# Optimization experiments

Measured on AMD Instinct MI355X. Metric: run time of the kernel, lower is better.

Reference implementation:

```python
import jax, jax.numpy as jnp
import numpy as np
import math

B, S, D, H = 4, 1024, 1024, 16
DK = D // H


def setup_inputs() -> dict:
    key = jax.random.key(0)
    ks = jax.random.split(key, 13)
    s = 1.0 / math.sqrt(D)
    inp = {
        "query": jax.random.normal(ks[0], (B, S, D), jnp.float32),
        "key": jax.random.normal(ks[1], (B, S, D), jnp.float32),
        "value": jax.random.normal(ks[2], (B, S, D), jnp.float32),
        "mask": jax.random.randint(ks[3], (B, S, S), 0, 2, jnp.int32),
        "wq": jax.random.normal(ks[4], (D, D), jnp.float32) * s,
        "bq": jax.random.normal(ks[5], (D,), jnp.float32) * s,
        "wk": jax.random.normal(ks[6], (D, D), jnp.float32) * s,
        "bk": jax.random.normal(ks[7], (D,), jnp.float32) * s,
        "wv": jax.random.normal(ks[8], (D, D), jnp.float32) * s,
        "bv": jax.random.normal(ks[9], (D,), jnp.float32) * s,
        "wo": jax.random.normal(ks[10], (D, D), jnp.float32) * s,
        "bo": jax.random.normal(ks[11], (D,), jnp.float32) * s,
    }
    return inp


def reference(query, key, value, mask, wq, bq, wk, bk, wv, bv, wo, bo):
    # QKV projections, split into heads: [B,S,D] -> [B,H,S,DK]
    def proj(x, w, b):
        return (x @ w.T + b).reshape(B, S, H, DK).transpose(0, 2, 1, 3)

    q = proj(query, wq, bq)
    k = proj(key, wk, bk)
    v = proj(value, wv, bv)

    scores = jnp.einsum("bhqd,bhkd->bhqk", q, k) / math.sqrt(DK)
    scores = scores + mask[:, None, :, :].astype(scores.dtype) * (-1e9)
    p = jax.nn.softmax(scores, axis=-1)
    x = jnp.einsum("bhqk,bhkd->bhqd", p, v)
    x = x.transpose(0, 2, 1, 3).reshape(B, S, D)
    # output projection (dropout is identity in eval)
    return x @ wo.T + bo
```

## Files before the change

kernel.cpp:

```cpp
#include <hip/hip_runtime.h>
#include <hip/hip_bf16.h>


typedef __bf16 bf16x8 __attribute__((ext_vector_type(8)));
typedef float f32x4 __attribute__((ext_vector_type(4)));
typedef unsigned short us8 __attribute__((ext_vector_type(8)));
typedef unsigned short us4 __attribute__((ext_vector_type(4)));

#define MFMA(a, b, c) __builtin_amdgcn_mfma_f32_16x16x32_bf16(a, b, c, 0, 0, 0)
#define EXP2(x) __builtin_amdgcn_exp2f(x)

__device__ __forceinline__ unsigned short f2b(float f) {
  return __builtin_bit_cast(unsigned short, __float2bfloat16(f));
}
__device__ __forceinline__ float b2f(unsigned short u) {
  return __builtin_bit_cast(float, (unsigned)u << 16);
}
__device__ __forceinline__ unsigned cvtpk(float lo, float hi) {
  unsigned r;
  asm("v_cvt_pk_bf16_f32 %0, %1, %2" : "=v"(r) : "v"(lo), "v"(hi));
  return r;
}
__device__ __forceinline__ bf16x8 ldbf8(const unsigned short* p) {
  return __builtin_bit_cast(bf16x8, *reinterpret_cast<const us8*>(p));
}
__device__ __forceinline__ us8 cvt8(float4 a, float4 b) {
  us8 o;
  o[0] = f2b(a.x); o[1] = f2b(a.y); o[2] = f2b(a.z); o[3] = f2b(a.w);
  o[4] = f2b(b.x); o[5] = f2b(b.y); o[6] = f2b(b.z); o[7] = f2b(b.w);
  return o;
}
__device__ __forceinline__ void glds16(const void* g, void* l) {
  __builtin_amdgcn_global_load_lds(
      (const __attribute__((address_space(1))) unsigned int*)g,
      (__attribute__((address_space(3))) unsigned int*)l, 16, 0, 0);
}

__global__ __launch_bounds__(256)
void prep(const float* __restrict__ query, const float* __restrict__ key,
          const float* __restrict__ value, const float* __restrict__ wq,
          const float* __restrict__ wk, const float* __restrict__ wv,
          unsigned short* __restrict__ Abfq, unsigned short* __restrict__ Abfk,
          unsigned short* __restrict__ Abfv, unsigned short* __restrict__ Wb) {
  const int bid = blockIdx.x, tid = threadIdx.x;
  const float* src;
  unsigned short* dst;
  size_t off;
  if (bid < 1536) {
    const int widx = bid >> 9;
    src = (widx == 0) ? wq : (widx == 1) ? wk : wv;
    dst = Wb + (size_t)widx * 1048576;
    off = (size_t)(bid & 511) * 2048 + tid * 8;
  } else if (bid < 3584) {
    src = query; dst = Abfq; off = (size_t)(bid - 1536) * 2048 + tid * 8;
  } else if (bid < 5632) {
    src = key; dst = Abfk; off = (size_t)(bid - 3584) * 2048 + tid * 8;
  } else {
    src = value; dst = Abfv; off = (size_t)(bid - 5632) * 2048 + tid * 8;
  }
  const float4* p = reinterpret_cast<const float4*>(src + off);
  *reinterpret_cast<us8*>(dst + off) = cvt8(p[0], p[1]);
}

__global__ __launch_bounds__(256)
void maskcvt(const int* __restrict__ mask, unsigned short* __restrict__ Mf) {
  const int idx = blockIdx.x * 256 + threadIdx.x;
  const int wl = idx & 63, tile = idx >> 6;
  const int kt = tile & 63, qt = (tile >> 6) & 63, b = tile >> 12;
  const int lr = wl & 15, lg = wl >> 4;
  const int4 mv = *reinterpret_cast<const int4*>(
      mask + (size_t)(b * 1024 + qt * 16 + lr) * 1024 + kt * 16 + lg * 4);
  us4 o;
  o[0] = mv.x ? 0xCEACu : 0xC1C0u;
  o[1] = mv.y ? 0xCEACu : 0xC1C0u;
  o[2] = mv.z ? 0xCEACu : 0xC1C0u;
  o[3] = mv.w ? 0xCEACu : 0xC1C0u;
  *reinterpret_cast<us4*>(Mf + (size_t)idx * 4) = o;
}

__global__ __launch_bounds__(256)
void cvt_w(const float* __restrict__ src, unsigned short* __restrict__ dst) {
  const size_t off = (size_t)blockIdx.x * 2048 + threadIdx.x * 8;
  const float4* p = reinterpret_cast<const float4*>(src + off);
  *reinterpret_cast<us8*>(dst + off) = cvt8(p[0], p[1]);
}

__global__ __launch_bounds__(256, 6)
void gemm_proj(const unsigned short* __restrict__ Aq,
               const unsigned short* __restrict__ Ak,
               const unsigned short* __restrict__ Av_bf,
               const float* __restrict__ Av_f32,
               const unsigned short* __restrict__ Wb,
               const float* __restrict__ bq, const float* __restrict__ bk,
               const float* __restrict__ bv, unsigned short* __restrict__ Qb,
               unsigned short* __restrict__ Kf, unsigned short* __restrict__ Vf,
               float qscale) {
  constexpr int K = 1024, N = 1024;
  __shared__ __align__(16) unsigned short As[2][128 * 32];
  __shared__ __align__(16) unsigned short Bs[2][64 * 32];
  const int lid = blockIdx.x + (blockIdx.y << 5) + (blockIdx.z << 9);
  const int xcd = lid & 7, slot = lid >> 3;
  const int chunk = ((slot >> 4) << 3) + xcd;
  const int z = chunk >> 5;
  const int bm = (chunk & 31) * 128;
  const int bn = (slot & 15) * 64;

  const unsigned short* Abf = (z == 0) ? Aq : (z == 1) ? Ak : Av_bf;
  const bool f32path = (z == 2) && (Av_bf == nullptr);
  const unsigned short* Bw = Wb + (size_t)z * 1048576;
  const float* bias = (z == 0) ? bq : (z == 1) ? bk : bv;
  const int t = threadIdx.x;
  const int w = t >> 6, lane = t & 63, lr = lane & 15, lg = lane >> 4;
  const int wr = w >> 1, wc = w & 1;

#define SWZ(row) ((((row) ^ ((row) >> 2)) & 3) << 4)

  f32x4 acc[4][2];
#pragma unroll
  for (int m = 0; m < 4; ++m)
#pragma unroll
    for (int n = 0; n < 2; ++n) acc[m][n] = f32x4{0.f, 0.f, 0.f, 0.f};

  auto stageA = [&](int k0, int buf) {
#pragma unroll
    for (int it = 0; it < 2; ++it) {
      const int s = it * 256 + t, row = s >> 2, cb = (s & 3) * 16;
      const char* g = (const char*)Abf + ((size_t)(bm + row) * 1024 + k0) * 2 +
                      (cb ^ SWZ(row));
      char* l = (char*)&As[buf][0] + (it * 256 + w * 64) * 16;
      glds16(g, l);
    }
  };
  auto stageB = [&](int k0, int buf) {
    const int row = t >> 2, cb = (t & 3) * 16;
    const char* g = (const char*)Bw + ((size_t)(bn + row) * 1024 + k0) * 2 +
                    (cb ^ SWZ(row));
    char* l = (char*)&Bs[buf][0] + (w * 64) * 16;
    glds16(g, l);
  };
#define STA8(buf, it, v)                                                       \
  {                                                                            \
    const int s_ = (it) * 256 + t, row_ = s_ >> 2, cb_ = (s_ & 3) * 16;        \
    *reinterpret_cast<us8*>((char*)&As[buf][0] + row_ * 64 +                   \
                            (cb_ ^ SWZ(row_))) = (v);                          \
  }

  if (f32path) {
#pragma unroll
    for (int it = 0; it < 2; ++it) {
      const int s = it * 256 + t, row = s >> 2, col = (s & 3) * 8;
      const float4* p =
          reinterpret_cast<const float4*>(Av_f32 + (size_t)(bm + row) * K + col);
      STA8(0, it, cvt8(p[0], p[1]));
    }
  } else {
    stageA(0, 0);
  }
  stageB(0, 0);
  __syncthreads();

  for (int c = 0; c < 32; ++c) {
    const int buf = c & 1;
    float4 fa[4];
    if (c < 31) {
      const int k1 = (c + 1) * 32;
      if (f32path) {
#pragma unroll
        for (int it = 0; it < 2; ++it) {
          const int s = it * 256 + t, row = s >> 2, col = (s & 3) * 8;
          const float4* p = reinterpret_cast<const float4*>(
              Av_f32 + (size_t)(bm + row) * K + k1 + col);
          fa[2 * it] = p[0];
          fa[2 * it + 1] = p[1];
        }
      } else {
        stageA(k1, buf ^ 1);
      }
      stageB(k1, buf ^ 1);
    }
    {
      bf16x8 af[4], bfr[2];
#pragma unroll
      for (int m = 0; m < 4; ++m) {
        const int row = wr * 64 + m * 16 + lr;
        af[m] = ldbf8((const unsigned short*)((char*)&As[buf][0] + row * 64 +
                                              ((lg * 16) ^ SWZ(row))));
      }
#pragma unroll
      for (int n = 0; n < 2; ++n) {
        const int row = wc * 32 + n * 16 + lr;
        bfr[n] = ldbf8((const unsigned short*)((char*)&Bs[buf][0] + row * 64 +
                                               ((lg * 16) ^ SWZ(row))));
      }
#pragma unroll
      for (int m = 0; m < 4; ++m)
#pragma unroll
        for (int n = 0; n < 2; ++n) acc[m][n] = MFMA(af[m], bfr[n], acc[m][n]);
    }
    if (c < 31 && f32path) {
#pragma unroll
      for (int it = 0; it < 2; ++it) STA8(buf ^ 1, it, cvt8(fa[2 * it], fa[2 * it + 1]));
    }
    __syncthreads();
  }
#undef STA8
#undef SWZ

#pragma unroll
  for (int m = 0; m < 4; ++m) {
    const int mr = bm + wr * 64 + m * 16 + lg * 4;
#pragma unroll
    for (int nt = 0; nt < 2; ++nt) {
      const int n = bn + wc * 32 + nt * 16 + lr;
      const float bb = bias[n];
      if (z == 0) {
#pragma unroll
        for (int r = 0; r < 4; ++r)
          Qb[(size_t)(mr + r) * N + n] = f2b((acc[m][nt][r] + bb) * qscale);
      } else if (z == 1) {
        const int b2 = mr >> 10, s0 = mr & 1023, hh = n >> 6, dd = n & 63;
        const size_t base = (size_t)(b2 * 16 + hh) * 65536 + (size_t)(dd >> 5) * 32768 +
                            (size_t)(s0 >> 4) * 512 +
                            (size_t)((s0 & 15) | (((dd >> 3) & 3) << 4)) * 8 + (dd & 7);
#pragma unroll
        for (int r = 0; r < 4; ++r) Kf[base + r * 8] = f2b(acc[m][nt][r] + bb);
      } else {
        const int b2 = mr >> 10, s0 = mr & 1023, hh = n >> 6, dd = n & 63;
        const size_t base = (size_t)(b2 * 16 + hh) * 65536 + (size_t)(s0 >> 5) * 2048 +
                            (size_t)(dd >> 4) * 512 +
                            (size_t)((dd & 15) | (((s0 >> 3) & 3) << 4)) * 8 + (s0 & 7);
        us4 pk;
#pragma unroll
        for (int r = 0; r < 4; ++r) pk[r] = f2b(acc[m][nt][r] + bb);
        *reinterpret_cast<us4*>(&Vf[base]) = pk;
      }
    }
  }
}

__global__ __launch_bounds__(256)
void gemm_out(const unsigned short* __restrict__ A, const unsigned short* __restrict__ Bw,
              const float* __restrict__ bias, float* __restrict__ Out) {
  constexpr int K = 1024, N = 1024;
  __shared__ __align__(16) unsigned short As[2][128 * 64];
  __shared__ __align__(16) unsigned short Bs[2][64 * 64];
  const int lid = blockIdx.x + (blockIdx.y << 5);
  const int xcd = lid & 7, slot = lid >> 3;
  const int chunk = ((slot >> 5) << 3) + xcd;
  const int pos = slot & 31;
  const int bm = ((chunk << 1) + (pos >> 4)) * 128;
  const int bn = (pos & 15) * 64;
  const int t = threadIdx.x;
  const int w = t >> 6, lane = t & 63, lr = lane & 15, lg = lane >> 4;
  const int wr = w >> 1, wc = w & 1;
  const int swzc = (lr & 7) << 4;

  f32x4 acc[4][2];
#pragma unroll
  for (int m = 0; m < 4; ++m)
#pragma unroll
    for (int n = 0; n < 2; ++n) acc[m][n] = f32x4{0.f, 0.f, 0.f, 0.f};

  auto stageA = [&](int k0, int buf) {
#pragma unroll
    for (int it = 0; it < 4; ++it) {
      const int s = it * 256 + t, row = s >> 3, cb = (s & 7) * 16;
      const char* g = (const char*)A + ((size_t)(bm + row) * 1024 + k0) * 2 +
                      (cb ^ ((row & 7) << 4));
      char* l = (char*)&As[buf][0] + (it * 256 + w * 64) * 16;
      glds16(g, l);
    }
  };
  auto stageB = [&](int k0, int buf) {
#pragma unroll
    for (int it = 0; it < 2; ++it) {
      const int s = it * 256 + t, row = s >> 3, cb = (s & 7) * 16;
      const char* g = (const char*)Bw + ((size_t)(bn + row) * 1024 + k0) * 2 +
                      (cb ^ ((row & 7) << 4));
      char* l = (char*)&Bs[buf][0] + (it * 256 + w * 64) * 16;
      glds16(g, l);
    }
  };

  stageA(0, 0);
  stageB(0, 0);
  __syncthreads();

  for (int c = 0; c < 16; ++c) {
    const int buf = c & 1;
    if (c < 15) {
      const int k1 = (c + 1) * 64;
      stageA(k1, buf ^ 1);
      stageB(k1, buf ^ 1);
    }
#pragma unroll
    for (int h2 = 0; h2 < 2; ++h2) {
      bf16x8 af[4], bfr[2];
#pragma unroll
      for (int m = 0; m < 4; ++m) {
        const int row = wr * 64 + m * 16 + lr;
        af[m] = ldbf8((const unsigned short*)((char*)&As[buf][0] + row * 128 +
                                              ((h2 * 64 + lg * 16) ^ swzc)));
      }
#pragma unroll
      for (int n = 0; n < 2; ++n) {
        const int row = wc * 32 + n * 16 + lr;
        bfr[n] = ldbf8((const unsigned short*)((char*)&Bs[buf][0] + row * 128 +
                                               ((h2 * 64 + lg * 16) ^ swzc)));
      }
#pragma unroll
      for (int m = 0; m < 4; ++m)
#pragma unroll
        for (int n = 0; n < 2; ++n) acc[m][n] = MFMA(af[m], bfr[n], acc[m][n]);
    }
    __syncthreads();
  }

#pragma unroll
  for (int m = 0; m < 4; ++m) {
    const int mr = bm + wr * 64 + m * 16 + lg * 4;
#pragma unroll
    for (int nt = 0; nt < 2; ++nt) {
      const int n = bn + wc * 32 + nt * 16 + lr;
      const float bb = bias[n];
#pragma unroll
      for (int r = 0; r < 4; ++r) Out[(size_t)(mr + r) * N + n] = acc[m][nt][r] + bb;
    }
  }
}

__global__ __launch_bounds__(256)
void attn_v7(const unsigned short* __restrict__ Qb,
             const unsigned short* __restrict__ Kf,
             const unsigned short* __restrict__ Vf,
             const unsigned short* __restrict__ Mf,
             unsigned short* __restrict__ ctx) {
  __shared__ __align__(16) unsigned short S[2][8192];
  __shared__ __align__(16) unsigned short sP[4][16 * 64];
  const int lid = blockIdx.x + (blockIdx.y << 6);
  const int xcd = lid & 7, slot = lid >> 3;
  const int bh = ((slot >> 4) << 3) + xcd;
  const int qb = slot & 15;
  const int b = bh >> 4, h = bh & 15;
  const int t = threadIdx.x, w = t >> 6, wl = t & 63, lr = wl & 15, lg = wl >> 4;
  const int q0 = qb * 64 + w * 16;
  const int swz = (lr & 7) << 4;

  const unsigned short* qp = Qb + (size_t)(b * 1024 + q0 + lr) * 1024 + h * 64 + lg * 8;
  const bf16x8 bq0 = ldbf8(qp);
  const bf16x8 bq1 = ldbf8(qp + 32);

  const unsigned short* KfB = Kf + (size_t)bh * 65536;
  const unsigned short* VfB = Vf + (size_t)bh * 65536;
  const unsigned short* mfp = Mf + (size_t)((b * 64 + qb * 4 + w) * 64) * 256 + wl * 4;

  f32x4 O[4];
  float l_ = 0.f;
#pragma unroll
  for (int dt = 0; dt < 4; ++dt) O[dt] = f32x4{0.f, 0.f, 0.f, 0.f};
  unsigned short* sp = &sP[w][0];

  auto stage = [&](int kc, int buf) {
    const unsigned short* srcs[4] = {KfB + kc * 2048, KfB + 32768 + kc * 2048,
                                     VfB + kc * 4096, VfB + kc * 4096 + 2048};
#pragma unroll
    for (int r = 0; r < 4; ++r) {
      const char* g = (const char*)(srcs[r] + (size_t)t * 8);
      char* l = (char*)&S[buf][r * 2048 + w * 512];
      glds16(g, l);
    }
  };

  stage(0, 0);
  __syncthreads();

  for (int kc = 0; kc < 16; ++kc) {
    const int buf = kc & 1;
    if (kc < 15) stage(kc + 1, buf ^ 1);

    us4 mk[4];
#pragma unroll
    for (int t4 = 0; t4 < 4; ++t4)
      mk[t4] = *reinterpret_cast<const us4*>(mfp + (size_t)(kc * 4 + t4) * 256);

    bf16x8 ak[4][2];
#pragma unroll
    for (int t4 = 0; t4 < 4; ++t4) {
      ak[t4][0] = ldbf8(&S[buf][t4 * 512 + wl * 8]);
      ak[t4][1] = ldbf8(&S[buf][2048 + t4 * 512 + wl * 8]);
    }

    f32x4 sc[4];
    __builtin_amdgcn_s_setprio(1);
#pragma unroll
    for (int t4 = 0; t4 < 4; ++t4) {
      f32x4 a;
#pragma unroll
      for (int r = 0; r < 4; ++r) a[r] = b2f(mk[t4][r]);
      a = MFMA(ak[t4][0], bq0, a);
      a = MFMA(ak[t4][1], bq1, a);
      sc[t4] = a;
    }
    __builtin_amdgcn_s_setprio(0);

    float ps = 0.f;
#pragma unroll
    for (int t4 = 0; t4 < 4; ++t4) {
      const float e0 = EXP2(sc[t4][0]), e1 = EXP2(sc[t4][1]);
      const float e2 = EXP2(sc[t4][2]), e3 = EXP2(sc[t4][3]);
      ps += (e0 + e1) + (e2 + e3);
      uint2 pw;
      pw.x = cvtpk(e0, e1);
      pw.y = cvtpk(e2, e3);
      *reinterpret_cast<uint2*>((char*)sp + lr * 128 + ((t4 * 32 + lg * 8) ^ swz)) = pw;
    }
    ps += __shfl_xor(ps, 16);
    ps += __shfl_xor(ps, 32);
    l_ += ps;

    __builtin_amdgcn_s_setprio(1);
#pragma unroll
    for (int ks = 0; ks < 2; ++ks) {
      bf16x8 ap =
          ldbf8((const unsigned short*)((char*)sp + lr * 128 + ((ks * 64 + lg * 16) ^ swz)));
#pragma unroll
      for (int dt = 0; dt < 4; ++dt) {
        bf16x8 bv = ldbf8(&S[buf][4096 + ks * 2048 + dt * 512 + wl * 8]);
        O[dt] = MFMA(ap, bv, O[dt]);
      }
    }
    __builtin_amdgcn_s_setprio(0);

    __syncthreads();
  }

  float linv[4];
#pragma unroll
  for (int r = 0; r < 4; ++r) linv[r] = 1.0f / __shfl(l_, lg * 4 + r);
#pragma unroll
  for (int dt = 0; dt < 4; ++dt)
#pragma unroll
    for (int r = 0; r < 4; ++r)
      ctx[(size_t)(b * 1024 + q0 + lg * 4 + r) * 1024 + h * 64 + dt * 16 + lr] =
          f2b(O[dt][r] * linv[r]);
}

extern "C" void kernel_launch(void* const* d_in, const int* in_sizes, int n_in,
                              void* d_out, int out_size, void* d_ws, size_t ws_size,
                              hipStream_t stream) {
  const float* query = (const float*)d_in[0];
  const float* key   = (const float*)d_in[1];
  const float* value = (const float*)d_in[2];
  const int*   mask  = (const int*)d_in[3];
  const float* wq = (const float*)d_in[4];
  const float* bq = (const float*)d_in[5];
  const float* wk = (const float*)d_in[6];
  const float* bk = (const float*)d_in[7];
  const float* wv = (const float*)d_in[8];
  const float* bv = (const float*)d_in[9];
  const float* wo = (const float*)d_in[10];
  const float* bo = (const float*)d_in[11];
  float* out = (float*)d_out;

  const size_t SZ = (size_t)4096 * 1024;
  unsigned short* Qb   = (unsigned short*)d_ws;
  unsigned short* Kf   = Qb + SZ;
  unsigned short* Vf   = Kf + SZ;
  unsigned short* ctx  = Vf + SZ;
  unsigned short* Abfq = (unsigned short*)d_out;
  unsigned short* Wb   = Abfq + SZ;
  unsigned short* Mf   = (unsigned short*)d_out;
  unsigned short* Abfk = ctx;
  const bool big = ws_size >= (size_t)40 * 1024 * 1024;
  unsigned short* Abfv = big ? (ctx + SZ) : nullptr;
  unsigned short* Wob  = Vf;

  const float qscale = 0.125f * 1.4426950408889634f;
  dim3 blk(256);
  prep<<<big ? 7680 : 5632, blk, 0, stream>>>(query, key, value, wq, wk, wv,
                                              Abfq, Abfk, Abfv, Wb);
  gemm_proj<<<dim3(32, 16, 3), blk, 0, stream>>>(Abfq, Abfk, Abfv, value, Wb,
                                                 bq, bk, bv, Qb, Kf, Vf, qscale);
  maskcvt<<<4096, blk, 0, stream>>>(mask, Mf);
  attn_v7<<<dim3(64, 16), blk, 0, stream>>>(Qb, Kf, Vf, Mf, ctx);
  cvt_w<<<512, blk, 0, stream>>>(wo, Wob);
  gemm_out<<<dim3(32, 16), blk, 0, stream>>>(ctx, Wob, bo, out);
}
```

Measured before the change: 127.3 us.

## Enlarge projection GEMM tile to 128x128 with 512-thread blocks

Changes the QKV projection GEMM from 128x64 tiles with 256 threads to 128x128 tiles with 512 threads (8 waves laid out 2x4). Each thread now stages one A and one B chunk per k-step, and the grid shrinks to 32x8x3 with the XCD-aware block mapping adjusted. The aim is more reuse of each staged A tile and fewer blocks re-reading A. In exchange, LDS per block doubles and there are half as many blocks, which may lower occupancy and load balance across CUs.

New measurement: 117.1 us. 1.09x faster.

```diff
diff --git a/kernel.cpp b/kernel.cpp
--- a/kernel.cpp
+++ b/kernel.cpp
@@ -85,7 +85,7 @@
   *reinterpret_cast<us8*>(dst + off) = cvt8(p[0], p[1]);
 }
 
-__global__ __launch_bounds__(256, 6)
+__global__ __launch_bounds__(512, 6)
 void gemm_proj(const unsigned short* __restrict__ Aq,
                const unsigned short* __restrict__ Ak,
                const unsigned short* __restrict__ Av_bf,
@@ -97,13 +97,13 @@
                float qscale) {
   constexpr int K = 1024, N = 1024;
   __shared__ __align__(16) unsigned short As[2][128 * 32];
-  __shared__ __align__(16) unsigned short Bs[2][64 * 32];
-  const int lid = blockIdx.x + (blockIdx.y << 5) + (blockIdx.z << 9);
+  __shared__ __align__(16) unsigned short Bs[2][128 * 32];
+  const int lid = blockIdx.x + (blockIdx.y << 5) + (blockIdx.z << 8);
   const int xcd = lid & 7, slot = lid >> 3;
-  const int chunk = ((slot >> 4) << 3) + xcd;
+  const int chunk = ((slot >> 3) << 3) + xcd;
   const int z = chunk >> 5;
   const int bm = (chunk & 31) * 128;
-  const int bn = (slot & 15) * 64;
+  const int bn = (slot & 7) * 128;
 
   const unsigned short* Abf = (z == 0) ? Aq : (z == 1) ? Ak : Av_bf;
   const bool f32path = (z == 2) && (Av_bf == nullptr);
@@ -111,7 +111,7 @@
   const float* bias = (z == 0) ? bq : (z == 1) ? bk : bv;
   const int t = threadIdx.x;
   const int w = t >> 6, lane = t & 63, lr = lane & 15, lg = lane >> 4;
-  const int wr = w >> 1, wc = w & 1;
+  const int wr = w >> 2, wc = w & 3;
 
 #define SWZ(row) ((((row) ^ ((row) >> 2)) & 3) << 4)
 
@@ -122,14 +122,11 @@
     for (int n = 0; n < 2; ++n) acc[m][n] = f32x4{0.f, 0.f, 0.f, 0.f};
 
   auto stageA = [&](int k0, int buf) {
-#pragma unroll
-    for (int it = 0; it < 2; ++it) {
-      const int s = it * 256 + t, row = s >> 2, cb = (s & 3) * 16;
-      const char* g = (const char*)Abf + ((size_t)(bm + row) * 1024 + k0) * 2 +
-                      (cb ^ SWZ(row));
-      char* l = (char*)&As[buf][0] + (it * 256 + w * 64) * 16;
-      glds16(g, l);
-    }
+    const int row = t >> 2, cb = (t & 3) * 16;
+    const char* g = (const char*)Abf + ((size_t)(bm + row) * 1024 + k0) * 2 +
+                    (cb ^ SWZ(row));
+    char* l = (char*)&As[buf][0] + (w * 64) * 16;
+    glds16(g, l);
   };
   auto stageB = [&](int k0, int buf) {
     const int row = t >> 2, cb = (t & 3) * 16;
@@ -138,21 +135,18 @@
     char* l = (char*)&Bs[buf][0] + (w * 64) * 16;
     glds16(g, l);
   };
-#define STA8(buf, it, v)                                                       \
+#define STA8(buf, v)                                                           \
   {                                                                            \
-    const int s_ = (it) * 256 + t, row_ = s_ >> 2, cb_ = (s_ & 3) * 16;        \
+    const int row_ = t >> 2, cb_ = (t & 3) * 16;                               \
     *reinterpret_cast<us8*>((char*)&As[buf][0] + row_ * 64 +                   \
                             (cb_ ^ SWZ(row_))) = (v);                          \
   }
 
   if (f32path) {
-#pragma unroll
-    for (int it = 0; it < 2; ++it) {
-      const int s = it * 256 + t, row = s >> 2, col = (s & 3) * 8;
-      const float4* p =
-          reinterpret_cast<const float4*>(Av_f32 + (size_t)(bm + row) * K + col);
-      STA8(0, it, cvt8(p[0], p[1]));
-    }
+    const int row = t >> 2, col = (t & 3) * 8;
+    const float4* p =
+        reinterpret_cast<const float4*>(Av_f32 + (size_t)(bm + row) * K + col);
+    STA8(0, cvt8(p[0], p[1]));
   } else {
     stageA(0, 0);
   }
@@ -161,18 +155,15 @@
 
   for (int c = 0; c < 32; ++c) {
     const int buf = c & 1;
-    float4 fa[4];
+    float4 fa[2];
     if (c < 31) {
       const int k1 = (c + 1) * 32;
       if (f32path) {
-#pragma unroll
-        for (int it = 0; it < 2; ++it) {
-          const int s = it * 256 + t, row = s >> 2, col = (s & 3) * 8;
-          const float4* p = reinterpret_cast<const float4*>(
-              Av_f32 + (size_t)(bm + row) * K + k1 + col);
-          fa[2 * it] = p[0];
-          fa[2 * it + 1] = p[1];
-        }
+        const int row = t >> 2, col = (t & 3) * 8;
+        const float4* p = reinterpret_cast<const float4*>(
+            Av_f32 + (size_t)(bm + row) * K + k1 + col);
+        fa[0] = p[0];
+        fa[1] = p[1];
       } else {
         stageA(k1, buf ^ 1);
       }
@@ -198,8 +189,7 @@
         for (int n = 0; n < 2; ++n) acc[m][n] = MFMA(af[m], bfr[n], acc[m][n]);
     }
     if (c < 31 && f32path) {
-#pragma unroll
-      for (int it = 0; it < 2; ++it) STA8(buf ^ 1, it, cvt8(fa[2 * it], fa[2 * it + 1]));
+      STA8(buf ^ 1, cvt8(fa[0], fa[1]));
     }
     __syncthreads();
   }
@@ -479,8 +469,8 @@
   dim3 blk(256);
   prep<<<big ? 7680 : 5632, blk, 0, stream>>>(query, key, value, wq, wk, wv,
                                               Abfq, Abfk, Abfv, Wb);
-  gemm_proj<<<dim3(32, 16, 3), blk, 0, stream>>>(Abfq, Abfk, Abfv, value, Wb,
-                                                 bq, bk, bv, Qb, Kf, Vf, qscale);
+  gemm_proj<<<dim3(32, 8, 3), dim3(512), 0, stream>>>(Abfq, Abfk, Abfv, value, Wb,
+                                                      bq, bk, bv, Qb, Kf, Vf, qscale);
   maskcvt<<<4096, blk, 0, stream>>>(mask, Mf);
   attn_v7<<<dim3(64, 16), blk, 0, stream>>>(Qb, Kf, Vf, Mf, ctx);
   cvt_w<<<512, blk, 0, stream>>>(wo, Wob);
```
